# Kernel optimization log

Measured on AMD Instinct MI355X. Metric: run time of the kernel, lower is better.

Reference implementation:

```python
import jax, jax.numpy as jnp
import numpy as np

DOWNSAMPLE = 512  # points per cloud, from init_kwargs


def _pairwise_dist(x, y):
    """Batched Euclidean distance matrix. x: (B,n,D), y: (B,m,D) -> (B,n,m)."""
    x2 = jnp.sum(x * x, axis=-1)                     # (B,n)
    y2 = jnp.sum(y * y, axis=-1)                     # (B,m)
    d2 = x2[:, :, None] + y2[:, None, :] - 2.0 * jnp.einsum('bnd,bmd->bnm', x, y)
    pos = d2 > 0.0                                   # guard sqrt(0)/negatives from fp error
    return jnp.where(pos, jnp.sqrt(jnp.where(pos, d2, 1.0)), 0.0)


def setup_inputs() -> dict:
    key = jax.random.key(0)
    k1, k2 = jax.random.split(key)
    inp = jax.random.normal(k1, (65536, 128), dtype=jnp.float32)
    tgt = jax.random.normal(k2, (65536, 128), dtype=jnp.float32)
    return {"input": inp, "target": tgt}


def reference(input, target):
    D = input.shape[-1]
    x = input.reshape(-1, DOWNSAMPLE, D)   # (B, n, D)
    y = target.reshape(-1, DOWNSAMPLE, D)  # (B, n, D)
    # geomloss energy kernel loss with uniform weights:
    # L_b = mean||x-y|| - 0.5*mean||x-x'|| - 0.5*mean||y-y'||
    cross = jnp.mean(_pairwise_dist(x, y), axis=(1, 2))  # (B,)
    xx = jnp.mean(_pairwise_dist(x, x), axis=(1, 2))
    yy = jnp.mean(_pairwise_dist(y, y), axis=(1, 2))
    loss = cross - 0.5 * xx - 0.5 * yy
    return jnp.mean(loss)
```

## Files before the change

### kernel.cpp

```cpp
#include <hip/hip_runtime.h>

typedef __attribute__((ext_vector_type(8))) __bf16 bf16x8;
typedef __attribute__((ext_vector_type(4))) float f32x4;
typedef __attribute__((ext_vector_type(8))) unsigned short ushort8;

#define DSAMP 512
#define DIM   128
#define S1    ((size_t)16777216)
#define REG5  16384
#define NBPB  36
#define NORM_OFF (2 * S1)
#define PART_OFF (2 * S1 + 524288)
#define WS_NEEDED (PART_OFF + (size_t)128 * NBPB * 4)

__global__ __launch_bounds__(256)
void presplit6(const float* __restrict__ x, const float* __restrict__ y,
               char* __restrict__ ws) {
    const size_t t = (size_t)blockIdx.x * 256 + threadIdx.x;
    const int jb = (int)(t & 7);
    const int c  = (int)((t >> 3) & 1);
    const int r  = (int)(t >> 4);
    const int input = r >> 16;
    const int ri    = r & 65535;

    const float* src = (input ? y : x) + ((size_t)ri << 7) + c * 64 + jb * 8;
    float4 v0 = ((const float4*)src)[0];
    float4 v1 = ((const float4*)src)[1];

    float s = v0.x * v0.x + v0.y * v0.y + v0.z * v0.z + v0.w * v0.w
            + v1.x * v1.x + v1.y * v1.y + v1.z * v1.z + v1.w * v1.w;
    #pragma unroll
    for (int o = 8; o > 0; o >>= 1) s += __shfl_down(s, o, 16);

    float xs[8] = {v0.x, v0.y, v0.z, v0.w, v1.x, v1.y, v1.z, v1.w};
    ushort8 hv;
    #pragma unroll
    for (int e = 0; e < 8; ++e) {
        unsigned ub = __float_as_uint(xs[e]);
        hv[e] = (unsigned short)((ub + 0x7fffu + ((ub >> 16) & 1u)) >> 16);
    }

    const int b  = ri >> 9;
    const int rb = ri & 511;
    char* hi = ws + (size_t)input * S1;
    size_t off = ((size_t)(b * 2 + c) * 512 + rb) * 128
               + (size_t)((jb ^ (rb & 7)) * 16);
    *(ushort8*)(hi + off) = hv;

    if ((t & 15) == 0) {
        float* nG = (float*)(ws + NORM_OFF) + (size_t)input * 65536;
        nG[ri] = s;
    }
}

__global__ __launch_bounds__(256, 4)
void mmd_tile9(const char* __restrict__ ws, float* __restrict__ partials) {
    __shared__ __align__(16) char smem[2 * REG5];
    __shared__ float Pn[128];
    __shared__ float Qn[128];
    __shared__ float wred[4];

    const int tid = threadIdx.x;
    const int xcd = blockIdx.x & 7;
    const int seq = blockIdx.x >> 3;
    const int b   = xcd + 8 * (seq / NBPB);
    const int s   = seq % NBPB;

    int type, ti, tj; float w; bool diag;
    if (s < 16) { type = 0; ti = s >> 2; tj = s & 3; w = 1.0f; diag = false; }
    else {
        int u = s - 16;
        type = 1 + (u >= 10);
        if (u >= 10) u -= 10;
        int i = (u >= 4) + (u >= 7) + (u >= 9);
        int off = (i == 1) ? 4 : (i == 2) ? 7 : (i == 3) ? 9 : 0;
        int j = u - off + i;
        ti = i; tj = j; diag = (i == j); w = diag ? -0.5f : -1.0f;
    }

    const char* Xhi = ws;
    const char* Yhi = ws + S1;
    const float* normX = (const float*)(ws + NORM_OFF);
    const float* normY = normX + 65536;

    const char* Phi = (type == 2) ? Yhi : Xhi;
    const char* Qhi = (type == 1) ? Xhi : Yhi;
    const float* nP = (type == 2) ? normY : normX;
    const float* nQ = (type == 1) ? normX : normY;

    if (tid < 128) Pn[tid]       = nP[(size_t)b * 512 + ti * 128 + tid];
    else           Qn[tid - 128] = nQ[(size_t)b * 512 + tj * 128 + (tid - 128)];

    const int lane    = tid & 63;
    const int wv      = tid >> 6;
    const int rowHalf = (wv >> 1) * 64;
    const int colHalf = (wv & 1) * 64;
    const int fm      = lane & 15;
    const int kq      = lane >> 4;
    const int sw      = fm & 7;

    f32x4 acc[4][4];
    #pragma unroll
    for (int a2 = 0; a2 < 4; ++a2)
        #pragma unroll
        for (int b2 = 0; b2 < 4; ++b2)
            acc[a2][b2] = (f32x4){0.f, 0.f, 0.f, 0.f};

    for (int c = 0; c < 2; ++c) {
        if (c) __syncthreads();
        size_t chrow = (size_t)(b * 2 + c) * 512;
        {
            const char* srcs[2];
            srcs[0] = Phi + (chrow + (size_t)ti * 128) * 128;
            srcs[1] = Qhi + (chrow + (size_t)tj * 128) * 128;
            #pragma unroll
            for (int f = 0; f < 8; ++f) {
                int g = wv * 8 + f;
                int region = g >> 4;
                int sub    = g & 15;
                const char* gs = srcs[region] + sub * 1024 + lane * 16;
                char* ls = smem + (size_t)region * REG5 + sub * 1024 + lane * 16;
                __builtin_amdgcn_global_load_lds(
                    (const __attribute__((address_space(1))) void*)gs,
                    (__attribute__((address_space(3))) void*)ls, 16, 0, 0);
            }
        }
        __syncthreads();
        #pragma unroll
        for (int ks = 0; ks < 2; ++ks) {
            const int jx = ((ks * 4 + kq) ^ sw) * 16;
            bf16x8 ah[4], bh[4];
            #pragma unroll
            for (int a2 = 0; a2 < 4; ++a2) {
                int ar = rowHalf + a2 * 16 + fm;
                ah[a2] = *(const bf16x8*)(smem + ar * 128 + jx);
            }
            #pragma unroll
            for (int b2 = 0; b2 < 4; ++b2) {
                int br = colHalf + b2 * 16 + fm;
                bh[b2] = *(const bf16x8*)(smem + REG5 + br * 128 + jx);
            }
            #pragma unroll
            for (int a2 = 0; a2 < 4; ++a2)
                #pragma unroll
                for (int b2 = 0; b2 < 4; ++b2)
                    acc[a2][b2] = __builtin_amdgcn_mfma_f32_16x16x32_bf16(ah[a2], bh[b2], acc[a2][b2], 0, 0, 0);
        }
    }

    float Pr[16], Qc[4];
    #pragma unroll
    for (int a2 = 0; a2 < 4; ++a2)
        #pragma unroll
        for (int rg = 0; rg < 4; ++rg)
            Pr[a2 * 4 + rg] = Pn[rowHalf + a2 * 16 + kq * 4 + rg];
    #pragma unroll
    for (int b2 = 0; b2 < 4; ++b2) Qc[b2] = Qn[colHalf + b2 * 16 + fm];

    float lsum = 0.f;
    if (diag) {
        #pragma unroll
        for (int a2 = 0; a2 < 4; ++a2)
            #pragma unroll
            for (int b2 = 0; b2 < 4; ++b2)
                #pragma unroll
                for (int rg = 0; rg < 4; ++rg) {
                    float d2 = fmaf(-2.0f, acc[a2][b2][rg], Pr[a2 * 4 + rg] + Qc[b2]);
                    float v  = __builtin_amdgcn_sqrtf(fmaxf(d2, 0.0f));
                    if ((rowHalf + a2 * 16 + kq * 4 + rg) == (colHalf + b2 * 16 + fm)) v = 0.f;
                    lsum += v;
                }
    } else {
        #pragma unroll
        for (int a2 = 0; a2 < 4; ++a2)
            #pragma unroll
            for (int b2 = 0; b2 < 4; ++b2)
                #pragma unroll
                for (int rg = 0; rg < 4; ++rg) {
                    float d2 = fmaf(-2.0f, acc[a2][b2][rg], Pr[a2 * 4 + rg] + Qc[b2]);
                    lsum += __builtin_amdgcn_sqrtf(fmaxf(d2, 0.0f));
                }
    }
    #pragma unroll
    for (int off = 32; off > 0; off >>= 1) lsum += __shfl_down(lsum, off, 64);
    if (lane == 0) wred[wv] = lsum;
    __syncthreads();
    if (tid == 0)
        partials[blockIdx.x] = (wred[0] + wred[1] + wred[2] + wred[3]) * w;
}

__global__ __launch_bounds__(256, 2)
void mmd_tile_fallback(const float* __restrict__ x, const float* __restrict__ y,
                       float* __restrict__ partials) {
    __shared__ __align__(16) char smem[4 * 128 * 144];
    __shared__ float Pn[128];
    __shared__ float Qn[128];
    __shared__ float wred[4];

    char* Ah = smem;
    char* Al = smem + 1 * 128 * 144;
    char* Bh = smem + 2 * 128 * 144;
    char* Bl = smem + 3 * 128 * 144;

    const int tid  = threadIdx.x;
    const int bid  = blockIdx.x;
    const int tj   = bid & 3;
    const int ti   = (bid >> 2) & 3;
    const int type = (bid >> 4) % 3;
    const int b    = bid / 48;

    const float* Xb = x + (size_t)b * DSAMP * DIM;
    const float* Yb = y + (size_t)b * DSAMP * DIM;
    const float* Pp; const float* Qp; float w;
    if (type == 0)      { Pp = Xb; Qp = Yb; w = 1.0f;  }
    else if (type == 1) { Pp = Xb; Qp = Xb; w = -0.5f; }
    else                { Pp = Yb; Qp = Yb; w = -0.5f; }
    Pp += (size_t)ti * 128 * DIM;
    Qp += (size_t)tj * 128 * DIM;

    {
        const float* rp = (tid < 128) ? (Pp + (size_t)tid * DIM)
                                      : (Qp + (size_t)(tid - 128) * DIM);
        float s = 0.f;
        #pragma unroll
        for (int k4 = 0; k4 < 32; ++k4) {
            float4 v = ((const float4*)rp)[k4];
            s += v.x * v.x + v.y * v.y + v.z * v.z + v.w * v.w;
        }
        if (tid < 128) Pn[tid] = s; else Qn[tid - 128] = s;
    }

    const int lane    = tid & 63;
    const int wv      = tid >> 6;
    const int rowHalf = (wv >> 1) * 64;
    const int colHalf = (wv & 1) * 64;
    const int fm      = lane & 15;
    const int kq      = lane >> 4;

    f32x4 acc[4][4];
    #pragma unroll
    for (int a2 = 0; a2 < 4; ++a2)
        #pragma unroll
        for (int b2 = 0; b2 < 4; ++b2)
            acc[a2][b2] = (f32x4){0.f, 0.f, 0.f, 0.f};

    for (int c = 0; c < 2; ++c) {
        if (c) __syncthreads();
        #pragma unroll
        for (int side = 0; side < 2; ++side) {
            const float* sp = side ? Qp : Pp;
            char* dh = side ? Bh : Ah;
            char* dl = side ? Bl : Al;
            #pragma unroll
            for (int it = 0; it < 4; ++it) {
                int u  = it * 256 + tid;
                int r  = u >> 3;
                int c8 = u & 7;
                const float* g = sp + (size_t)r * DIM + c * 64 + c8 * 8;
                float4 v0 = ((const float4*)g)[0];
                float4 v1 = ((const float4*)g)[1];
                float xs[8] = {v0.x, v0.y, v0.z, v0.w, v1.x, v1.y, v1.z, v1.w};
                ushort8 hv, lv;
                #pragma unroll
                for (int e = 0; e < 8; ++e) {
                    float xv = xs[e];
                    unsigned ub = __float_as_uint(xv);
                    unsigned hr = (ub + 0x7fffu + ((ub >> 16) & 1u)) >> 16;
                    float hf = __uint_as_float(hr << 16);
                    float rs = xv - hf;
                    unsigned ul = __float_as_uint(rs);
                    unsigned lr = (ul + 0x7fffu + ((ul >> 16) & 1u)) >> 16;
                    hv[e] = (unsigned short)hr;
                    lv[e] = (unsigned short)lr;
                }
                *(ushort8*)(dh + r * 144 + c8 * 16) = hv;
                *(ushort8*)(dl + r * 144 + c8 * 16) = lv;
            }
        }
        __syncthreads();
        #pragma unroll
        for (int ks = 0; ks < 2; ++ks) {
            const int kb2 = (ks * 32 + kq * 8) * 2;
            bf16x8 ah[4], al[4], bh[4], bl[4];
            #pragma unroll
            for (int a2 = 0; a2 < 4; ++a2) {
                int ar = rowHalf + a2 * 16 + fm;
                ah[a2] = *(const bf16x8*)(Ah + ar * 144 + kb2);
                al[a2] = *(const bf16x8*)(Al + ar * 144 + kb2);
            }
            #pragma unroll
            for (int b2 = 0; b2 < 4; ++b2) {
                int br = colHalf + b2 * 16 + fm;
                bh[b2] = *(const bf16x8*)(Bh + br * 144 + kb2);
                bl[b2] = *(const bf16x8*)(Bl + br * 144 + kb2);
            }
            #pragma unroll
            for (int a2 = 0; a2 < 4; ++a2)
                #pragma unroll
                for (int b2 = 0; b2 < 4; ++b2) {
                    acc[a2][b2] = __builtin_amdgcn_mfma_f32_16x16x32_bf16(ah[a2], bh[b2], acc[a2][b2], 0, 0, 0);
                    acc[a2][b2] = __builtin_amdgcn_mfma_f32_16x16x32_bf16(ah[a2], bl[b2], acc[a2][b2], 0, 0, 0);
                    acc[a2][b2] = __builtin_amdgcn_mfma_f32_16x16x32_bf16(al[a2], bh[b2], acc[a2][b2], 0, 0, 0);
                }
        }
    }

    const bool selfm = (type != 0) && (ti == tj);
    float lsum = 0.f;
    #pragma unroll
    for (int a2 = 0; a2 < 4; ++a2) {
        int ib = rowHalf + a2 * 16 + kq * 4;
        #pragma unroll
        for (int b2 = 0; b2 < 4; ++b2) {
            int j = colHalf + b2 * 16 + fm;
            float qn = Qn[j];
            #pragma unroll
            for (int rg = 0; rg < 4; ++rg) {
                int i = ib + rg;
                float d2 = Pn[i] + qn - 2.0f * acc[a2][b2][rg];
                if (d2 > 0.f && !(selfm && i == j)) lsum += sqrtf(d2);
            }
        }
    }
    #pragma unroll
    for (int off = 32; off > 0; off >>= 1) lsum += __shfl_down(lsum, off, 64);
    if (lane == 0) wred[wv] = lsum;
    __syncthreads();
    if (tid == 0)
        partials[bid] = (wred[0] + wred[1] + wred[2] + wred[3]) * w;
}

__global__ __launch_bounds__(256)
void mmd_finalize_kernel(const float* __restrict__ partials, int n,
                         float* __restrict__ out, double scale) {
    __shared__ double sh[256];
    double s = 0.0;
    for (int i = threadIdx.x; i < n; i += 256) s += (double)partials[i];
    sh[threadIdx.x] = s;
    __syncthreads();
    for (int off = 128; off > 0; off >>= 1) {
        if ((int)threadIdx.x < off) sh[threadIdx.x] += sh[threadIdx.x + off];
        __syncthreads();
    }
    if (threadIdx.x == 0) out[0] = (float)(sh[0] * scale);
}

extern "C" void kernel_launch(void* const* d_in, const int* in_sizes, int n_in,
                              void* d_out, int out_size, void* d_ws, size_t ws_size,
                              hipStream_t stream) {
    const float* x = (const float*)d_in[0];
    const float* y = (const float*)d_in[1];
    float* out = (float*)d_out;

    const int n = in_sizes[0];
    const int B = n / (DSAMP * DIM);
    const double scale = 1.0 / ((double)B * (double)DSAMP * (double)DSAMP);

    if (ws_size >= WS_NEEDED) {
        char* ws = (char*)d_ws;
        float* partials = (float*)(ws + PART_OFF);
        const int nblocks = B * NBPB;
        presplit6<<<dim3((2 * n / 8) / 256), dim3(256), 0, stream>>>(x, y, ws);
        mmd_tile9<<<dim3(nblocks), dim3(256), 0, stream>>>(ws, partials);
        mmd_finalize_kernel<<<dim3(1), dim3(256), 0, stream>>>(partials, nblocks, out, scale);
    } else {
        float* partials = (float*)d_ws;
        const int nblocks = B * 48;
        mmd_tile_fallback<<<dim3(nblocks), dim3(256), 0, stream>>>(x, y, partials);
        mmd_finalize_kernel<<<dim3(1), dim3(256), 0, stream>>>(partials, nblocks, out, scale);
    }
}
```

Before: 132.8 us.

## Pair two output tiles per block sharing the A panel, reorder presplit by XCD

Each block now computes two 128x128 distance tiles that share the same A row panel. Pairings come from constant lookup tables, which halves the block count and reuses the staged A data across both tiles. The loop stages the B panels one at a time in a third LDS region, so more shared memory is used and occupancy drops to 3 blocks per CU. The presplit kernel is also remapped so each XCD handles the clouds its tile blocks will read, and the batch index order is reversed for L2 locality. The fast path is now restricted to B==128.

```diff
diff --git a/kernel.cpp b/kernel.cpp
--- a/kernel.cpp
+++ b/kernel.cpp
@@ -9,19 +9,28 @@
 #define S1    ((size_t)16777216)
 #define REG5  16384
 #define NBPB  36
+#define NPAIR 18
 #define NORM_OFF (2 * S1)
 #define PART_OFF (2 * S1 + 524288)
 #define WS_NEEDED (PART_OFF + (size_t)128 * NBPB * 4)
 
 __global__ __launch_bounds__(256)
-void presplit6(const float* __restrict__ x, const float* __restrict__ y,
+void presplit7(const float* __restrict__ x, const float* __restrict__ y,
                char* __restrict__ ws) {
-    const size_t t = (size_t)blockIdx.x * 256 + threadIdx.x;
-    const int jb = (int)(t & 7);
-    const int c  = (int)((t >> 3) & 1);
-    const int r  = (int)(t >> 4);
-    const int input = r >> 16;
-    const int ri    = r & 65535;
+    const int bid = blockIdx.x;
+    const int xcd = bid & 7;
+    const int q   = bid >> 3;
+    const int bi  = q >> 6;
+    const int rem = q & 63;
+    const int input = rem >> 5;
+    const int rg  = rem & 31;
+    const int b   = xcd + 8 * bi;
+
+    const int tid = threadIdx.x;
+    const int jb  = tid & 7;
+    const int c   = (tid >> 3) & 1;
+    const int rb  = rg * 16 + (tid >> 4);
+    const int ri  = b * 512 + rb;
 
     const float* src = (input ? y : x) + ((size_t)ri << 7) + c * 64 + jb * 8;
     float4 v0 = ((const float4*)src)[0];
@@ -40,56 +49,67 @@
         hv[e] = (unsigned short)((ub + 0x7fffu + ((ub >> 16) & 1u)) >> 16);
     }
 
-    const int b  = ri >> 9;
-    const int rb = ri & 511;
     char* hi = ws + (size_t)input * S1;
     size_t off = ((size_t)(b * 2 + c) * 512 + rb) * 128
                + (size_t)((jb ^ (rb & 7)) * 16);
     *(ushort8*)(hi + off) = hv;
 
-    if ((t & 15) == 0) {
+    if ((tid & 15) == 0) {
         float* nG = (float*)(ws + NORM_OFF) + (size_t)input * 65536;
         nG[ri] = s;
     }
 }
 
-__global__ __launch_bounds__(256, 4)
-void mmd_tile9(const char* __restrict__ ws, float* __restrict__ partials) {
-    __shared__ __align__(16) char smem[2 * REG5];
+__constant__ unsigned char T_Asrc[NPAIR]  = {0,0,0,0,0,0,0,0, 1,1,1,1,1,1,1,1,1,1};
+__constant__ unsigned char T_Ai[NPAIR]    = {0,0,1,1,1,2,2,3, 0,0,0,0,1,1,1,2,2,3};
+__constant__ unsigned char T_Bsrc0[NPAIR] = {0,0,0,0,1,0,1,0, 1,1,0,0,1,1,0,1,0,1};
+__constant__ unsigned char T_Bsrc1[NPAIR] = {0,0,0,1,1,0,1,1, 1,1,0,0,1,0,0,1,0,0};
+__constant__ unsigned char T_Bj0[NPAIR]   = {0,2,1,3,2,2,2,3, 0,2,0,2,1,3,2,2,0,3};
+__constant__ unsigned char T_Bj1[NPAIR]   = {1,3,2,1,3,3,3,3, 1,3,1,3,2,0,3,3,3,0};
+__constant__ char          T_wc0[NPAIR]   = {2,1,2,1,0,2,0,2, 2,1,0,0,2,1,0,2,0,2};
+__constant__ char          T_wc1[NPAIR]   = {1,1,1,0,0,1,0,0, 1,1,0,0,1,0,0,1,0,0};
+__constant__ unsigned char T_d0[NPAIR]    = {1,0,1,0,0,1,0,1, 1,0,0,0,1,0,0,1,0,1};
+
+__global__ __launch_bounds__(256, 3)
+void mmd_pair(const char* __restrict__ ws, float* __restrict__ partials) {
+    __shared__ __align__(16) char smem[3 * REG5];
     __shared__ float Pn[128];
-    __shared__ float Qn[128];
+    __shared__ float Qn0[128];
+    __shared__ float Qn1[128];
     __shared__ float wred[4];
 
-    const int tid = threadIdx.x;
-    const int xcd = blockIdx.x & 7;
-    const int seq = blockIdx.x >> 3;
-    const int b   = xcd + 8 * (seq / NBPB);
-    const int s   = seq % NBPB;
-
-    int type, ti, tj; float w; bool diag;
-    if (s < 16) { type = 0; ti = s >> 2; tj = s & 3; w = 1.0f; diag = false; }
-    else {
-        int u = s - 16;
-        type = 1 + (u >= 10);
-        if (u >= 10) u -= 10;
-        int i = (u >= 4) + (u >= 7) + (u >= 9);
-        int off = (i == 1) ? 4 : (i == 2) ? 7 : (i == 3) ? 9 : 0;
-        int j = u - off + i;
-        ti = i; tj = j; diag = (i == j); w = diag ? -0.5f : -1.0f;
-    }
-
-    const char* Xhi = ws;
-    const char* Yhi = ws + S1;
+    const int tid  = threadIdx.x;
+    const int bid  = blockIdx.x;
+    const int xcd  = bid & 7;
+    const int seq  = bid >> 3;
+    const int s    = seq % NPAIR;
+    const int bseq = seq / NPAIR;
+    const int b    = xcd + 8 * (15 - bseq);
+
     const float* normX = (const float*)(ws + NORM_OFF);
     const float* normY = normX + 65536;
 
-    const char* Phi = (type == 2) ? Yhi : Xhi;
-    const char* Qhi = (type == 1) ? Xhi : Yhi;
-    const float* nP = (type == 2) ? normY : normX;
-    const float* nQ = (type == 1) ? normX : normY;
-
-    if (tid < 128) Pn[tid]       = nP[(size_t)b * 512 + ti * 128 + tid];
-    else           Qn[tid - 128] = nQ[(size_t)b * 512 + tj * 128 + (tid - 128)];
+    const int Ai  = T_Ai[s];
+    const int Bj0 = T_Bj0[s];
+    const int Bj1 = T_Bj1[s];
+    const char* Ap  = ws + (T_Asrc[s]  ? S1 : 0);
+    const char* Bp0 = ws + (T_Bsrc0[s] ? S1 : 0);
+    const char* Bp1 = ws + (T_Bsrc1[s] ? S1 : 0);
+    const float* nA  = T_Asrc[s]  ? normY : normX;
+    const float* nB0 = T_Bsrc0[s] ? normY : normX;
+    const float* nB1 = T_Bsrc1[s] ? normY : normX;
+    const int wc0 = T_wc0[s], wc1 = T_wc1[s];
+    const float w0 = (wc0 == 0) ? 1.0f : ((wc0 == 1) ? -1.0f : -0.5f);
+    const float w1 = (wc1 == 0) ? 1.0f : ((wc1 == 1) ? -1.0f : -0.5f);
+    const bool dg0 = T_d0[s] != 0;
+
+    if (tid < 128) {
+        Pn[tid] = nA[(size_t)b * 512 + Ai * 128 + tid];
+    } else {
+        int qn = tid - 128;
+        Qn0[qn] = nB0[(size_t)b * 512 + Bj0 * 128 + qn];
+        Qn1[qn] = nB1[(size_t)b * 512 + Bj1 * 128 + qn];
+    }
 
     const int lane    = tid & 63;
     const int wv      = tid >> 6;
@@ -99,94 +119,131 @@
     const int kq      = lane >> 4;
     const int sw      = fm & 7;
 
+    const size_t ch0 = (size_t)(b * 2 + 0) * 512;
+    const size_t ch1 = (size_t)(b * 2 + 1) * 512;
+
+    {
+        const char* sA0 = Ap  + (ch0 + (size_t)Ai  * 128) * 128;
+        const char* sA1 = Ap  + (ch1 + (size_t)Ai  * 128) * 128;
+        const char* sB  = Bp0 + (ch0 + (size_t)Bj0 * 128) * 128;
+        #pragma unroll
+        for (int f = 0; f < 12; ++f) {
+            int g = wv * 12 + f;
+            const char* base = (g < 16) ? sA0 : ((g < 32) ? sA1 : sB);
+            const char* gs = base + (g & 15) * 1024 + lane * 16;
+            char* ls = smem + (size_t)g * 1024 + lane * 16;
+            __builtin_amdgcn_global_load_lds(
+                (const __attribute__((address_space(1))) void*)gs,
+                (__attribute__((address_space(3))) void*)ls, 16, 0, 0);
+        }
+    }
+
+    auto stageB = [&](const char* Bp, int Bj, size_t ch) {
+        const char* src = Bp + (ch + (size_t)Bj * 128) * 128;
+        #pragma unroll
+        for (int f = 0; f < 4; ++f) {
+            int g = wv * 4 + f;
+            const char* gs = src + g * 1024 + lane * 16;
+            char* ls = smem + 2 * REG5 + (size_t)g * 1024 + lane * 16;
+            __builtin_amdgcn_global_load_lds(
+                (const __attribute__((address_space(1))) void*)gs,
+                (__attribute__((address_space(3))) void*)ls, 16, 0, 0);
+        }
+    };
+
     f32x4 acc[4][4];
-    #pragma unroll
-    for (int a2 = 0; a2 < 4; ++a2)
-        #pragma unroll
-        for (int b2 = 0; b2 < 4; ++b2)
-            acc[a2][b2] = (f32x4){0.f, 0.f, 0.f, 0.f};
-
-    for (int c = 0; c < 2; ++c) {
-        if (c) __syncthreads();
-        size_t chrow = (size_t)(b * 2 + c) * 512;
-        {
-            const char* srcs[2];
-            srcs[0] = Phi + (chrow + (size_t)ti * 128) * 128;
-            srcs[1] = Qhi + (chrow + (size_t)tj * 128) * 128;
-            #pragma unroll
-            for (int f = 0; f < 8; ++f) {
-                int g = wv * 8 + f;
-                int region = g >> 4;
-                int sub    = g & 15;
-                const char* gs = srcs[region] + sub * 1024 + lane * 16;
-                char* ls = smem + (size_t)region * REG5 + sub * 1024 + lane * 16;
-                __builtin_amdgcn_global_load_lds(
-                    (const __attribute__((address_space(1))) void*)gs,
-                    (__attribute__((address_space(3))) void*)ls, 16, 0, 0);
-            }
-        }
-        __syncthreads();
+    auto zero_acc = [&]() {
+        #pragma unroll
+        for (int a2 = 0; a2 < 4; ++a2)
+            #pragma unroll
+            for (int b2 = 0; b2 < 4; ++b2)
+                acc[a2][b2] = (f32x4){0.f, 0.f, 0.f, 0.f};
+    };
+
+    auto compute = [&](int creg) {
+        const char* Ab = smem + creg * REG5;
+        const char* Bb = smem + 2 * REG5;
         #pragma unroll
         for (int ks = 0; ks < 2; ++ks) {
             const int jx = ((ks * 4 + kq) ^ sw) * 16;
             bf16x8 ah[4], bh[4];
             #pragma unroll
-            for (int a2 = 0; a2 < 4; ++a2) {
-                int ar = rowHalf + a2 * 16 + fm;
-                ah[a2] = *(const bf16x8*)(smem + ar * 128 + jx);
-            }
-            #pragma unroll
-            for (int b2 = 0; b2 < 4; ++b2) {
-                int br = colHalf + b2 * 16 + fm;
-                bh[b2] = *(const bf16x8*)(smem + REG5 + br * 128 + jx);
-            }
+            for (int a2 = 0; a2 < 4; ++a2)
+                ah[a2] = *(const bf16x8*)(Ab + (rowHalf + a2 * 16 + fm) * 128 + jx);
+            #pragma unroll
+            for (int b2 = 0; b2 < 4; ++b2)
+                bh[b2] = *(const bf16x8*)(Bb + (colHalf + b2 * 16 + fm) * 128 + jx);
             #pragma unroll
             for (int a2 = 0; a2 < 4; ++a2)
                 #pragma unroll
                 for (int b2 = 0; b2 < 4; ++b2)
-                    acc[a2][b2] = __builtin_amdgcn_mfma_f32_16x16x32_bf16(ah[a2], bh[b2], acc[a2][b2], 0, 0, 0);
-        }
-    }
-
-    float Pr[16], Qc[4];
-    #pragma unroll
-    for (int a2 = 0; a2 < 4; ++a2)
-        #pragma unroll
-        for (int rg = 0; rg < 4; ++rg)
-            Pr[a2 * 4 + rg] = Pn[rowHalf + a2 * 16 + kq * 4 + rg];
-    #pragma unroll
-    for (int b2 = 0; b2 < 4; ++b2) Qc[b2] = Qn[colHalf + b2 * 16 + fm];
-
-    float lsum = 0.f;
-    if (diag) {
+                    acc[a2][b2] = __builtin_amdgcn_mfma_f32_16x16x32_bf16(
+                        ah[a2], bh[b2], acc[a2][b2], 0, 0, 0);
+        }
+    };
+
+    auto tile_sum = [&](const float* Qn, bool dg) -> float {
+        float Pr[16], Qc[4];
         #pragma unroll
         for (int a2 = 0; a2 < 4; ++a2)
             #pragma unroll
-            for (int b2 = 0; b2 < 4; ++b2)
+            for (int rg2 = 0; rg2 < 4; ++rg2)
+                Pr[a2 * 4 + rg2] = Pn[rowHalf + a2 * 16 + kq * 4 + rg2];
+        #pragma unroll
+        for (int b2 = 0; b2 < 4; ++b2) Qc[b2] = Qn[colHalf + b2 * 16 + fm];
+        float ls = 0.f;
+        if (dg) {
+            #pragma unroll
+            for (int a2 = 0; a2 < 4; ++a2)
                 #pragma unroll
-                for (int rg = 0; rg < 4; ++rg) {
-                    float d2 = fmaf(-2.0f, acc[a2][b2][rg], Pr[a2 * 4 + rg] + Qc[b2]);
-                    float v  = __builtin_amdgcn_sqrtf(fmaxf(d2, 0.0f));
-                    if ((rowHalf + a2 * 16 + kq * 4 + rg) == (colHalf + b2 * 16 + fm)) v = 0.f;
-                    lsum += v;
-                }
-    } else {
-        #pragma unroll
-        for (int a2 = 0; a2 < 4; ++a2)
-            #pragma unroll
-            for (int b2 = 0; b2 < 4; ++b2)
+                for (int b2 = 0; b2 < 4; ++b2)
+                    #pragma unroll
+                    for (int rg2 = 0; rg2 < 4; ++rg2) {
+                        float d2 = fmaf(-2.0f, acc[a2][b2][rg2], Pr[a2 * 4 + rg2] + Qc[b2]);
+                        float v  = __builtin_amdgcn_sqrtf(fmaxf(d2, 0.0f));
+                        if ((rowHalf + a2 * 16 + kq * 4 + rg2) == (colHalf + b2 * 16 + fm)) v = 0.f;
+                        ls += v;
+                    }
+        } else {
+            #pragma unroll
+            for (int a2 = 0; a2 < 4; ++a2)
                 #pragma unroll
-                for (int rg = 0; rg < 4; ++rg) {
-                    float d2 = fmaf(-2.0f, acc[a2][b2][rg], Pr[a2 * 4 + rg] + Qc[b2]);
-                    lsum += __builtin_amdgcn_sqrtf(fmaxf(d2, 0.0f));
-                }
-    }
+                for (int b2 = 0; b2 < 4; ++b2)
+                    #pragma unroll
+                    for (int rg2 = 0; rg2 < 4; ++rg2) {
+                        float d2 = fmaf(-2.0f, acc[a2][b2][rg2], Pr[a2 * 4 + rg2] + Qc[b2]);
+                        ls += __builtin_amdgcn_sqrtf(fmaxf(d2, 0.0f));
+                    }
+        }
+        return ls;
+    };
+
+    zero_acc();
+    __syncthreads();
+    compute(0);
+    __syncthreads();
+    stageB(Bp0, Bj0, ch1);
+    __syncthreads();
+    compute(1);
+    __syncthreads();
+    stageB(Bp1, Bj1, ch0);
+    float lsum = w0 * tile_sum(Qn0, dg0);
+    __syncthreads();
+
+    zero_acc();
+    compute(0);
+    __syncthreads();
+    stageB(Bp1, Bj1, ch1);
+    __syncthreads();
+    compute(1);
+    lsum += w1 * tile_sum(Qn1, false);
+
     #pragma unroll
     for (int off = 32; off > 0; off >>= 1) lsum += __shfl_down(lsum, off, 64);
     if (lane == 0) wred[wv] = lsum;
     __syncthreads();
     if (tid == 0)
-        partials[blockIdx.x] = (wred[0] + wred[1] + wred[2] + wred[3]) * w;
+        partials[bid] = wred[0] + wred[1] + wred[2] + wred[3];
 }
 
 __global__ __launch_bounds__(256, 2)
@@ -356,12 +413,12 @@
     const int B = n / (DSAMP * DIM);
     const double scale = 1.0 / ((double)B * (double)DSAMP * (double)DSAMP);
 
-    if (ws_size >= WS_NEEDED) {
+    if (ws_size >= WS_NEEDED && B == 128) {
         char* ws = (char*)d_ws;
         float* partials = (float*)(ws + PART_OFF);
-        const int nblocks = B * NBPB;
-        presplit6<<<dim3((2 * n / 8) / 256), dim3(256), 0, stream>>>(x, y, ws);
-        mmd_tile9<<<dim3(nblocks), dim3(256), 0, stream>>>(ws, partials);
+        const int nblocks = B * NPAIR;
+        presplit7<<<dim3(8192), dim3(256), 0, stream>>>(x, y, ws);
+        mmd_pair<<<dim3(nblocks), dim3(256), 0, stream>>>(ws, partials);
         mmd_finalize_kernel<<<dim3(1), dim3(256), 0, stream>>>(partials, nblocks, out, scale);
     } else {
         float* partials = (float*)d_ws;
```

Result: faster. 128.3 us (-3.4%).
